# Kernel optimization log

Hardware: AMD Instinct MI355X
Metric: run time of the kernel (lower is better)

Reference implementation:

```python
import jax, jax.numpy as jnp
import numpy as np


def setup_inputs() -> dict:
    key = jax.random.key(0)
    k1, k2 = jax.random.split(key)
    B, C, H, W = 8, 64, 128, 256
    left_feature = jax.random.normal(k1, (B, C, H, W), dtype=jnp.float32)
    right_feature = jax.random.normal(k2, (B, C, H, W), dtype=jnp.float32)
    return {
        "left_feature": left_feature,
        "right_feature": right_feature,
        "max_disp": 64,
    }


def reference(left_feature, right_feature, max_disp):
    # Stereo correlation cost volume (norm=False branch):
    #   volume[b, d, h, w] = mean_c( left[b,c,h,w] * right[b,c,h,w-d] )  for w >= d
    #   volume[b, d, h, w] = 0                                           for w <  d
    b, c, h, w = left_feature.shape

    def corr_at_disp(d):
        # left[:, :, :, d:] * right[:, :, :, :w-d], mean over channel dim
        prod = left_feature[:, :, :, d:] * right_feature[:, :, :, : w - d]
        cv = jnp.mean(prod, axis=1)  # (b, h, w-d)
        # left-pad along width with zeros for invalid disparities
        return jnp.pad(cv, ((0, 0), (0, 0), (d, 0)))

    # max_disp is a static Python int; loop over disparity hyperparameter is static.
    volume = jnp.stack([corr_at_disp(d) for d in range(max_disp)], axis=1)
    return volume  # (b, max_disp, h, w)
```

## Files before the change

### kernel.cpp

```cpp
#include <hip/hip_runtime.h>

typedef _Float16 half8 __attribute__((ext_vector_type(8)));
typedef float floatx4 __attribute__((ext_vector_type(4)));

#define BB 8
#define CC 64
#define HH 128
#define WW 256
#define DD 64
#define OPITCH 36

__global__ __launch_bounds__(64, 3)
void corr_volume_mfma(const float* __restrict__ left,
                      const float* __restrict__ right,
                      float* __restrict__ out) {
    __shared__ alignas(16) unsigned char smem[16384];
    _Float16* const Lb = (_Float16*)smem;
    _Float16* const Rb = (_Float16*)(smem + 4096);
    float*    const Ob = (float*)smem;

    const int lane = threadIdx.x;

    const int tsk = (blockIdx.x & 7) * 1024 + (blockIdx.x >> 3);
    const int bh  = tsk >> 3;
    const int W0  = (tsk & 7) * 32;
    const int b   = bh >> 7;
    const int h   = bh & 127;

    const size_t chanStride = (size_t)HH * WW;
    const size_t rowBase = (size_t)b * CC * chanStride + (size_t)h * WW;

    const int cg = lane >> 3;
    const int wq = (lane & 7) * 4;

    const float* lp = left  + rowBase + (size_t)(cg * 8) * chanStride;
    const float* rp = right + rowBase + (size_t)(cg * 8) * chanStride;

    float4 lv[8], ra[8], rbv[8];

    #pragma unroll
    for (int c = 0; c < 8; ++c)
        lv[c] = *(const float4*)(lp + (size_t)c * chanStride + (W0 + wq));
    #pragma unroll
    for (int c = 0; c < 8; ++c)
        ra[c] = *(const float4*)(rp + (size_t)c * chanStride + (W0 + wq));

    if (W0 < 64) {
        const int nz8 = (64 - W0) * 8;
        half8 z = {0, 0, 0, 0, 0, 0, 0, 0};
        for (int zz = lane; zz < nz8; zz += 64)
            *(half8*)&Rb[zz * 8] = z;
    }

    {
        const float* lf = (const float*)lv;
        #pragma unroll
        for (int s = 0; s < 4; ++s) {
            const int j   = wq + s;
            const int col = (cg ^ (j & 7)) * 8;
            half8 v;
            #pragma unroll
            for (int c = 0; c < 8; ++c) v[c] = (_Float16)lf[c * 4 + s];
            *(half8*)&Lb[j * 64 + col] = v;
        }
    }

    if (W0 >= 32) {
        #pragma unroll
        for (int c = 0; c < 8; ++c)
            rbv[c] = *(const float4*)(rp + (size_t)c * chanStride + (W0 - 32 + wq));
    }

    {
        const float* rf = (const float*)ra;
        #pragma unroll
        for (int s = 0; s < 4; ++s) {
            const int j   = 64 + wq + s;
            const int col = (cg ^ (j & 7)) * 8;
            half8 v;
            #pragma unroll
            for (int c = 0; c < 8; ++c) v[c] = (_Float16)rf[c * 4 + s];
            *(half8*)&Rb[j * 64 + col] = v;
        }
    }

    if (W0 >= 64) {
        #pragma unroll
        for (int c = 0; c < 8; ++c)
            ra[c] = *(const float4*)(rp + (size_t)c * chanStride + (W0 - 64 + wq));
    }

    if (W0 >= 32) {
        const float* rf = (const float*)rbv;
        #pragma unroll
        for (int s = 0; s < 4; ++s) {
            const int j   = 32 + wq + s;
            const int col = (cg ^ (j & 7)) * 8;
            half8 v;
            #pragma unroll
            for (int c = 0; c < 8; ++c) v[c] = (_Float16)rf[c * 4 + s];
            *(half8*)&Rb[j * 64 + col] = v;
        }
    }

    if (W0 >= 64) {
        const float* rf = (const float*)ra;
        #pragma unroll
        for (int s = 0; s < 4; ++s) {
            const int j   = wq + s;
            const int col = (cg ^ (j & 7)) * 8;
            half8 v;
            #pragma unroll
            for (int c = 0; c < 8; ++c) v[c] = (_Float16)rf[c * 4 + s];
            *(half8*)&Rb[j * 64 + col] = v;
        }
    }

    __syncthreads();

    const int n = lane & 15;
    const int q = lane >> 4;
    const float scale = 1.0f / 64.0f;

    floatx4 acc[2][5];
    #pragma unroll
    for (int tt = 0; tt < 2; ++tt)
        #pragma unroll
        for (int u = 0; u < 5; ++u)
            #pragma unroll
            for (int r = 0; r < 4; ++r)
                acc[tt][u][r] = 0.0f;

    #pragma unroll
    for (int kk = 0; kk < 2; ++kk) {
        const int col = ((kk * 4 + q) ^ (n & 7)) * 8;
        half8 bfrag[2], afrag[6];
        #pragma unroll
        for (int tt = 0; tt < 2; ++tt)
            bfrag[tt] = *(const half8*)&Lb[(tt * 16 + n) * 64 + col];
        #pragma unroll
        for (int a = 0; a < 6; ++a)
            afrag[a] = *(const half8*)&Rb[(a * 16 + n) * 64 + col];
        #pragma unroll
        for (int tt = 0; tt < 2; ++tt)
            #pragma unroll
            for (int u = 0; u < 5; ++u)
                acc[tt][u] = __builtin_amdgcn_mfma_f32_16x16x32_f16(
                    afrag[tt + u], bfrag[tt], acc[tt][u], 0, 0, 0);
    }

    __syncthreads();

    #pragma unroll
    for (int tt = 0; tt < 2; ++tt) {
        const int wloc = tt * 16 + n;
        #pragma unroll
        for (int u = 0; u < 5; ++u) {
            #pragma unroll
            for (int r = 0; r < 4; ++r) {
                const int d = 64 - 16 * u + n - (q * 4 + r);
                if (d >= 0 && d < DD) {
                    Ob[d * OPITCH + wloc] = acc[tt][u][r] * scale;
                }
            }
        }
    }

    __syncthreads();

    #pragma unroll
    for (int ii = 0; ii < 8; ++ii) {
        const int d    = ii * 8 + (lane >> 3);
        const int wloc = (lane & 7) * 4;
        const float4 v = *(const float4*)&Ob[d * OPITCH + wloc];
        *(float4*)&out[(((size_t)b * DD + d) * HH + h) * WW + W0 + wloc] = v;
    }
}

extern "C" void kernel_launch(void* const* d_in, const int* in_sizes, int n_in,
                              void* d_out, int out_size, void* d_ws, size_t ws_size,
                              hipStream_t stream) {
    const float* left  = (const float*)d_in[0];
    const float* right = (const float*)d_in[1];
    float* out = (float*)d_out;

    dim3 grid(8192);
    dim3 block(64);
    corr_volume_mfma<<<grid, block, 0, stream>>>(left, right, out);
}
```

Measured before the change: 184.8 us.

## Switch to persistent 512-thread blocks looping over row tiles with nontemporal stores

Measured after the change: 182.4 us. Within noise of the previous version (-1.3%).

```diff
diff --git a/kernel.cpp b/kernel.cpp
--- a/kernel.cpp
+++ b/kernel.cpp
@@ -8,24 +8,27 @@
 #define HH 128
 #define WW 256
 #define DD 64
+#define GRID 256
 #define OPITCH 36
 
-__global__ __launch_bounds__(64, 3)
+__global__ __launch_bounds__(512, 2)
 void corr_volume_mfma(const float* __restrict__ left,
                       const float* __restrict__ right,
                       float* __restrict__ out) {
-    __shared__ alignas(16) unsigned char smem[16384];
-    _Float16* const Lb = (_Float16*)smem;
-    _Float16* const Rb = (_Float16*)(smem + 4096);
-    float*    const Ob = (float*)smem;
+    __shared__ alignas(16) unsigned char smem[131072];
 
-    const int lane = threadIdx.x;
+    const int tid  = threadIdx.x;
+    const int lane = tid & 63;
+    const int wv   = tid >> 6;
 
-    const int tsk = (blockIdx.x & 7) * 1024 + (blockIdx.x >> 3);
-    const int bh  = tsk >> 3;
-    const int W0  = (tsk & 7) * 32;
-    const int b   = bh >> 7;
-    const int h   = bh & 127;
+    _Float16* const Lw = (_Float16*)(smem + wv * 16384);
+    _Float16* const Rw = (_Float16*)(smem + wv * 16384 + 4096);
+    float*    const Ob = (float*)(smem + wv * 16384);
+
+    const int bh   = blockIdx.x + (wv >> 1) * GRID;
+    const int b    = bh >> 7;
+    const int h    = bh & 127;
+    const int half = wv & 1;
 
     const size_t chanStride = (size_t)HH * WW;
     const size_t rowBase = (size_t)b * CC * chanStride + (size_t)h * WW;
@@ -33,147 +36,141 @@
     const int cg = lane >> 3;
     const int wq = (lane & 7) * 4;
 
-    const float* lp = left  + rowBase + (size_t)(cg * 8) * chanStride;
-    const float* rp = right + rowBase + (size_t)(cg * 8) * chanStride;
-
-    float4 lv[8], ra[8], rbv[8];
-
-    #pragma unroll
-    for (int c = 0; c < 8; ++c)
-        lv[c] = *(const float4*)(lp + (size_t)c * chanStride + (W0 + wq));
-    #pragma unroll
-    for (int c = 0; c < 8; ++c)
-        ra[c] = *(const float4*)(rp + (size_t)c * chanStride + (W0 + wq));
-
-    if (W0 < 64) {
-        const int nz8 = (64 - W0) * 8;
-        half8 z = {0, 0, 0, 0, 0, 0, 0, 0};
-        for (int zz = lane; zz < nz8; zz += 64)
-            *(half8*)&Rb[zz * 8] = z;
-    }
-
-    {
-        const float* lf = (const float*)lv;
-        #pragma unroll
-        for (int s = 0; s < 4; ++s) {
-            const int j   = wq + s;
-            const int col = (cg ^ (j & 7)) * 8;
-            half8 v;
-            #pragma unroll
-            for (int c = 0; c < 8; ++c) v[c] = (_Float16)lf[c * 4 + s];
-            *(half8*)&Lb[j * 64 + col] = v;
-        }
-    }
-
-    if (W0 >= 32) {
-        #pragma unroll
-        for (int c = 0; c < 8; ++c)
-            rbv[c] = *(const float4*)(rp + (size_t)c * chanStride + (W0 - 32 + wq));
-    }
-
-    {
-        const float* rf = (const float*)ra;
-        #pragma unroll
-        for (int s = 0; s < 4; ++s) {
-            const int j   = 64 + wq + s;
-            const int col = (cg ^ (j & 7)) * 8;
-            half8 v;
-            #pragma unroll
-            for (int c = 0; c < 8; ++c) v[c] = (_Float16)rf[c * 4 + s];
-            *(half8*)&Rb[j * 64 + col] = v;
-        }
-    }
-
-    if (W0 >= 64) {
-        #pragma unroll
-        for (int c = 0; c < 8; ++c)
-            ra[c] = *(const float4*)(rp + (size_t)c * chanStride + (W0 - 64 + wq));
-    }
-
-    if (W0 >= 32) {
-        const float* rf = (const float*)rbv;
-        #pragma unroll
-        for (int s = 0; s < 4; ++s) {
-            const int j   = 32 + wq + s;
-            const int col = (cg ^ (j & 7)) * 8;
-            half8 v;
-            #pragma unroll
-            for (int c = 0; c < 8; ++c) v[c] = (_Float16)rf[c * 4 + s];
-            *(half8*)&Rb[j * 64 + col] = v;
-        }
-    }
-
-    if (W0 >= 64) {
-        const float* rf = (const float*)ra;
-        #pragma unroll
-        for (int s = 0; s < 4; ++s) {
-            const int j   = wq + s;
-            const int col = (cg ^ (j & 7)) * 8;
-            half8 v;
-            #pragma unroll
-            for (int c = 0; c < 8; ++c) v[c] = (_Float16)rf[c * 4 + s];
-            *(half8*)&Rb[j * 64 + col] = v;
-        }
-    }
-
-    __syncthreads();
+    const float* lpb = left  + rowBase + (size_t)(cg * 8) * chanStride + wq;
+    const float* rpb = right + rowBase + (size_t)(cg * 8) * chanStride + wq;
 
     const int n = lane & 15;
     const int q = lane >> 4;
     const float scale = 1.0f / 64.0f;
 
-    floatx4 acc[2][5];
-    #pragma unroll
-    for (int tt = 0; tt < 2; ++tt)
+    #pragma unroll 1
+    for (int t = 0; t < 4; ++t) {
+        const int W0 = half * 128 + t * 32;
+
+        float4 lv[8], ra[8], rbv[8], rx[8];
         #pragma unroll
-        for (int u = 0; u < 5; ++u)
+        for (int c = 0; c < 8; ++c)
+            lv[c] = *(const float4*)(lpb + (size_t)c * chanStride + W0);
+        #pragma unroll
+        for (int c = 0; c < 8; ++c)
+            ra[c] = *(const float4*)(rpb + (size_t)c * chanStride + W0);
+        if (W0 >= 32) {
             #pragma unroll
-            for (int r = 0; r < 4; ++r)
-                acc[tt][u][r] = 0.0f;
+            for (int c = 0; c < 8; ++c)
+                rbv[c] = *(const float4*)(rpb + (size_t)c * chanStride + (W0 - 32));
+        }
+        if (W0 >= 64) {
+            #pragma unroll
+            for (int c = 0; c < 8; ++c)
+                rx[c] = *(const float4*)(rpb + (size_t)c * chanStride + (W0 - 64));
+        }
 
-    #pragma unroll
-    for (int kk = 0; kk < 2; ++kk) {
-        const int col = ((kk * 4 + q) ^ (n & 7)) * 8;
-        half8 bfrag[2], afrag[6];
-        #pragma unroll
-        for (int tt = 0; tt < 2; ++tt)
-            bfrag[tt] = *(const half8*)&Lb[(tt * 16 + n) * 64 + col];
-        #pragma unroll
-        for (int a = 0; a < 6; ++a)
-            afrag[a] = *(const half8*)&Rb[(a * 16 + n) * 64 + col];
+        if (W0 < 64) {
+            const int nz8 = (64 - W0) * 8;
+            half8 z = {0, 0, 0, 0, 0, 0, 0, 0};
+            for (int zz = lane; zz < nz8; zz += 64)
+                *(half8*)&Rw[zz * 8] = z;
+        }
+
+        {
+            const float* lf = (const float*)lv;
+            #pragma unroll
+            for (int s = 0; s < 4; ++s) {
+                const int j   = wq + s;
+                const int col = (cg ^ (j & 7)) * 8;
+                half8 v;
+                #pragma unroll
+                for (int c = 0; c < 8; ++c) v[c] = (_Float16)lf[c * 4 + s];
+                *(half8*)&Lw[j * 64 + col] = v;
+            }
+        }
+        {
+            const float* rf = (const float*)ra;
+            #pragma unroll
+            for (int s = 0; s < 4; ++s) {
+                const int j   = 64 + wq + s;
+                const int col = (cg ^ (j & 7)) * 8;
+                half8 v;
+                #pragma unroll
+                for (int c = 0; c < 8; ++c) v[c] = (_Float16)rf[c * 4 + s];
+                *(half8*)&Rw[j * 64 + col] = v;
+            }
+        }
+        if (W0 >= 32) {
+            const float* rf = (const float*)rbv;
+            #pragma unroll
+            for (int s = 0; s < 4; ++s) {
+                const int j   = 32 + wq + s;
+                const int col = (cg ^ (j & 7)) * 8;
+                half8 v;
+                #pragma unroll
+                for (int c = 0; c < 8; ++c) v[c] = (_Float16)rf[c * 4 + s];
+                *(half8*)&Rw[j * 64 + col] = v;
+            }
+        }
+        if (W0 >= 64) {
+            const float* rf = (const float*)rx;
+            #pragma unroll
+            for (int s = 0; s < 4; ++s) {
+                const int j   = wq + s;
+                const int col = (cg ^ (j & 7)) * 8;
+                half8 v;
+                #pragma unroll
+                for (int c = 0; c < 8; ++c) v[c] = (_Float16)rf[c * 4 + s];
+                *(half8*)&Rw[j * 64 + col] = v;
+            }
+        }
+
+        floatx4 acc[2][5];
         #pragma unroll
         for (int tt = 0; tt < 2; ++tt)
             #pragma unroll
             for (int u = 0; u < 5; ++u)
-                acc[tt][u] = __builtin_amdgcn_mfma_f32_16x16x32_f16(
-                    afrag[tt + u], bfrag[tt], acc[tt][u], 0, 0, 0);
-    }
+                #pragma unroll
+                for (int r = 0; r < 4; ++r)
+                    acc[tt][u][r] = 0.0f;
 
-    __syncthreads();
+        #pragma unroll
+        for (int kk = 0; kk < 2; ++kk) {
+            const int col = ((kk * 4 + q) ^ (n & 7)) * 8;
+            half8 bfrag[2], afrag[6];
+            #pragma unroll
+            for (int tt = 0; tt < 2; ++tt)
+                bfrag[tt] = *(const half8*)&Lw[(tt * 16 + n) * 64 + col];
+            #pragma unroll
+            for (int a = 0; a < 6; ++a)
+                afrag[a] = *(const half8*)&Rw[(a * 16 + n) * 64 + col];
+            #pragma unroll
+            for (int tt = 0; tt < 2; ++tt)
+                #pragma unroll
+                for (int u = 0; u < 5; ++u)
+                    acc[tt][u] = __builtin_amdgcn_mfma_f32_16x16x32_f16(
+                        afrag[tt + u], bfrag[tt], acc[tt][u], 0, 0, 0);
+        }
 
-    #pragma unroll
-    for (int tt = 0; tt < 2; ++tt) {
-        const int wloc = tt * 16 + n;
         #pragma unroll
-        for (int u = 0; u < 5; ++u) {
+        for (int tt = 0; tt < 2; ++tt) {
+            const int wloc = tt * 16 + n;
             #pragma unroll
-            for (int r = 0; r < 4; ++r) {
-                const int d = 64 - 16 * u + n - (q * 4 + r);
-                if (d >= 0 && d < DD) {
-                    Ob[d * OPITCH + wloc] = acc[tt][u][r] * scale;
+            for (int u = 0; u < 5; ++u) {
+                #pragma unroll
+                for (int r = 0; r < 4; ++r) {
+                    const int d = 64 - 16 * u + n - (q * 4 + r);
+                    if (d >= 0 && d < DD) {
+                        Ob[d * OPITCH + wloc] = acc[tt][u][r] * scale;
+                    }
                 }
             }
         }
-    }
 
-    __syncthreads();
-
-    #pragma unroll
-    for (int ii = 0; ii < 8; ++ii) {
-        const int d    = ii * 8 + (lane >> 3);
-        const int wloc = (lane & 7) * 4;
-        const float4 v = *(const float4*)&Ob[d * OPITCH + wloc];
-        *(float4*)&out[(((size_t)b * DD + d) * HH + h) * WW + W0 + wloc] = v;
+        #pragma unroll
+        for (int ii = 0; ii < 8; ++ii) {
+            const int d    = ii * 8 + (lane >> 3);
+            const int wloc = (lane & 7) * 4;
+            const floatx4 v = *(const floatx4*)&Ob[d * OPITCH + wloc];
+            floatx4* dst = (floatx4*)&out[(((size_t)b * DD + d) * HH + h) * WW + W0 + wloc];
+            __builtin_nontemporal_store(v, dst);
+        }
     }
 }
 
@@ -184,7 +181,7 @@
     const float* right = (const float*)d_in[1];
     float* out = (float*)d_out;
 
-    dim3 grid(8192);
-    dim3 block(64);
+    dim3 grid(GRID);
+    dim3 block(512);
     corr_volume_mfma<<<grid, block, 0, stream>>>(left, right, out);
 }
```
